# Optimization experiments

Hardware: AMD Instinct MI355X
Metric: run time of the kernel (lower is better)

The kernel has to match this reference:

```python
import jax, jax.numpy as jnp
import numpy as np

HEADS = 16
DIM = 1024
SPARSITY = 0.1


def setup_inputs() -> dict:
    key = jax.random.key(0)
    k1, k2, k3 = jax.random.split(key, 3)
    b, n, d = 2, 2048, DIM
    inner = HEADS * 64  # dim_head=64 -> inner_dim = 1024
    x = jax.random.normal(k1, (b, n, d), dtype=jnp.float32)
    W_qkv = jax.random.normal(k2, (3 * inner, d), dtype=jnp.float32) * (d ** -0.5)
    W_out = jax.random.normal(k3, (d, inner), dtype=jnp.float32) * (inner ** -0.5)
    b_out = jnp.zeros((d,), dtype=jnp.float32)
    return {"x": x, "W_qkv": W_qkv, "W_out": W_out, "b_out": b_out}


def reference(x, W_qkv, W_out, b_out):
    b, n, d = x.shape
    h = HEADS
    scale = d ** -0.5  # source uses dim**-0.5, not dim_head
    qkv = jnp.einsum('bnd,ed->bne', x, W_qkv)        # [b, n, 3*inner]
    q, k, v = jnp.split(qkv, 3, axis=-1)
    # b n (h dh) -> b h n dh
    def to_heads(t):
        return t.reshape(b, n, h, -1).transpose(0, 2, 1, 3)
    q, k, v = to_heads(q), to_heads(k), to_heads(v)
    dots = jnp.einsum('bhid,bhjd->bhij', q, k) * scale  # [b, h, n, n]
    mask_value = -jnp.finfo(dots.dtype).max
    k_top = max(1, int(SPARSITY * n))
    topk_vals, _ = jax.lax.top_k(dots, k_top)           # [b, h, n, k_top]
    thresh = topk_vals[..., -1:]                         # kth largest per row
    dots = jnp.where(dots >= thresh, dots, mask_value)   # keep ties, like torch
    v = jax.nn.relu(v)
    attn = jax.nn.softmax(dots, axis=-1)
    out = jnp.einsum('bhij,bhjd->bhid', attn, v)         # [b, h, n, dh]
    out = out.transpose(0, 2, 1, 3).reshape(b, n, -1)    # [b, n, inner]
    out = jnp.einsum('bne,de->bnd', out, W_out) + b_out  # to_out Linear (dropout=0)
    return out
```

## Files before the change

### kernel.cpp

```cpp
#include <hip/hip_runtime.h>


using f16x8 = __attribute__((ext_vector_type(8))) _Float16;
using u16x8 = __attribute__((ext_vector_type(8))) unsigned short;
using f32x4 = __attribute__((ext_vector_type(4))) float;

#define MFMA16F(a, b, c) __builtin_amdgcn_mfma_f32_16x16x32_f16(a, b, c, 0, 0, 0)

__device__ __forceinline__ unsigned short f2h(float f) {
  return __builtin_bit_cast(unsigned short, (_Float16)f);
}
__device__ __forceinline__ float h2f(unsigned int u) {
  return (float)__builtin_bit_cast(_Float16, (unsigned short)u);
}
__device__ __forceinline__ unsigned int key16(unsigned int u) {
  return (u & 0x8000u) ? (~u & 0xFFFFu) : (u | 0x8000u);
}
__device__ __forceinline__ unsigned int inv_key16(unsigned int k) {
  return (k & 0x8000u) ? (k & 0x7FFFu) : (~k & 0xFFFFu);
}
__device__ __forceinline__ float wred_sum(float v) {
#pragma unroll
  for (int off = 32; off > 0; off >>= 1) v += __shfl_xor(v, off);
  return v;
}

__device__ __forceinline__ int hist_select(const unsigned int* hw, int lane,
                                           int rank, int* cntAbove) {
  unsigned int S = hw[4 * lane] + hw[4 * lane + 1] + hw[4 * lane + 2] + hw[4 * lane + 3];
#pragma unroll
  for (int off = 1; off < 64; off <<= 1) {
    unsigned int v = (unsigned int)__shfl_down((int)S, off);
    if (lane + off < 64) S += v;
  }
  unsigned long long ball = __ballot((int)S >= rank);
  int lstar = 63 - __builtin_clzll(ball);
  unsigned int Sst = (unsigned int)__shfl((int)S, lstar);
  unsigned int h0 = hw[4 * lstar], h1 = hw[4 * lstar + 1];
  unsigned int h2 = hw[4 * lstar + 2], h3 = hw[4 * lstar + 3];
  unsigned int g = Sst - h0 - h1 - h2 - h3;
  int bb; unsigned int ca;
  if ((int)(g + h3) >= rank)                { bb = 4 * lstar + 3; ca = g; }
  else if ((int)(g + h3 + h2) >= rank)      { bb = 4 * lstar + 2; ca = g + h3; }
  else if ((int)(g + h3 + h2 + h1) >= rank) { bb = 4 * lstar + 1; ca = g + h3 + h2; }
  else                                      { bb = 4 * lstar;     ca = g + h3 + h2 + h1; }
  *cntAbove = (int)ca;
  return bb;
}

__global__ void cast_f32_f16(const float* __restrict__ s,
                             unsigned short* __restrict__ d, int n4, int scaleN4) {
  int i = blockIdx.x * blockDim.x + threadIdx.x;
  int stride = gridDim.x * blockDim.x;
  for (; i < n4; i += stride) {
    float4 v = ((const float4*)s)[i];
    float sc = (i < scaleN4) ? 0.03125f : 1.0f;
    ushort4 o;
    o.x = f2h(v.x * sc); o.y = f2h(v.y * sc); o.z = f2h(v.z * sc); o.w = f2h(v.w * sc);
    ((ushort4*)d)[i] = o;
  }
}

__global__ __launch_bounds__(256, 2) void gemm_qkv(
    const unsigned short* __restrict__ A, const unsigned short* __restrict__ W,
    unsigned short* __restrict__ out) {
  const int K = 1024;
  __shared__ unsigned short As[128 * 32];
  __shared__ unsigned short Bs[128 * 32];
  int t = threadIdx.x;
  int m0 = blockIdx.y * 128, n0 = blockIdx.x * 128;
  int lane = t & 63, wave = t >> 6;
  int wm = wave >> 1, wn = wave & 1;
  int rs = t >> 2, cs = t & 3;
  int cl = cs ^ ((rs >> 1) & 3);
  const unsigned short* pa0 = A + (size_t)(m0 + rs) * K + cl * 8;
  const unsigned short* pa1 = A + (size_t)(m0 + rs + 64) * K + cl * 8;
  const unsigned short* pb0 = W + (size_t)(n0 + rs) * K + cl * 8;
  const unsigned short* pb1 = W + (size_t)(n0 + rs + 64) * K + cl * 8;
  u16x8 ra0 = *(const u16x8*)pa0;
  u16x8 ra1 = *(const u16x8*)pa1;
  u16x8 rb0 = *(const u16x8*)pb0;
  u16x8 rb1 = *(const u16x8*)pb1;
  f32x4 zz = {0.f, 0.f, 0.f, 0.f};
  f32x4 acc[4][4];
#pragma unroll
  for (int i = 0; i < 4; ++i)
#pragma unroll
    for (int j = 0; j < 4; ++j) acc[i][j] = zz;
  int rr = lane & 15, cc = lane >> 4;
  int slot = (cc ^ ((rr >> 1) & 3)) * 8;
  for (int kt = 0; kt < K; kt += 32) {
    __syncthreads();
    *(u16x8*)&As[rs * 32 + cs * 8] = ra0;
    *(u16x8*)&As[(rs + 64) * 32 + cs * 8] = ra1;
    *(u16x8*)&Bs[rs * 32 + cs * 8] = rb0;
    *(u16x8*)&Bs[(rs + 64) * 32 + cs * 8] = rb1;
    if (kt + 32 < K) {
      ra0 = *(const u16x8*)(pa0 + kt + 32);
      ra1 = *(const u16x8*)(pa1 + kt + 32);
      rb0 = *(const u16x8*)(pb0 + kt + 32);
      rb1 = *(const u16x8*)(pb1 + kt + 32);
    }
    __syncthreads();
    f16x8 af[4], bfr[4];
#pragma unroll
    for (int f = 0; f < 4; ++f) {
      af[f]  = *(const f16x8*)&As[(wm * 64 + f * 16 + rr) * 32 + slot];
      bfr[f] = *(const f16x8*)&Bs[(wn * 64 + f * 16 + rr) * 32 + slot];
    }
#pragma unroll
    for (int fi = 0; fi < 4; ++fi)
#pragma unroll
      for (int fj = 0; fj < 4; ++fj)
        acc[fi][fj] = MFMA16F(bfr[fj], af[fi], acc[fi][fj]);
  }
#pragma unroll
  for (int fi = 0; fi < 4; ++fi) {
#pragma unroll
    for (int fj = 0; fj < 4; ++fj) {
      int m = m0 + wm * 64 + fi * 16 + rr;
      int n = n0 + wn * 64 + fj * 16 + cc * 4;
      ushort4 pk;
      pk.x = f2h(acc[fi][fj][0]); pk.y = f2h(acc[fi][fj][1]);
      pk.z = f2h(acc[fi][fj][2]); pk.w = f2h(acc[fi][fj][3]);
      *(ushort4*)&out[(size_t)m * 3072 + n] = pk;
    }
  }
}

__global__ __launch_bounds__(256) void vtrans(const unsigned short* __restrict__ qkv,
                                              unsigned short* __restrict__ vt) {
  __shared__ unsigned short tile[64][72];
  int q0 = blockIdx.x * 64;
  int bh = blockIdx.y;
  int b = bh >> 4, h = bh & 15;
  int t = threadIdx.x;
  int r = t >> 2, seg = t & 3;
  const unsigned short* src =
      qkv + (size_t)(b * 2048 + q0 + r) * 3072 + 2048 + h * 64 + seg * 16;
  *(u16x8*)&tile[r][seg * 16]     = *(const u16x8*)src;
  *(u16x8*)&tile[r][seg * 16 + 8] = *(const u16x8*)(src + 8);
  __syncthreads();
  int dh = t & 63, qs = t >> 6;
  unsigned short vals[16];
#pragma unroll
  for (int j = 0; j < 16; ++j) {
    unsigned short v = tile[qs * 16 + j][dh];
    vals[j] = (v & 0x8000) ? (unsigned short)0 : v;
  }
  unsigned short* dst = vt + (size_t)(bh * 64 + dh) * 2048 + q0 + qs * 16;
  *(u16x8*)&dst[0] = *(u16x8*)&vals[0];
  *(u16x8*)&dst[8] = *(u16x8*)&vals[8];
}

#define DSF 2068
__global__ __launch_bounds__(512, 4) void attn3(
    const unsigned short* __restrict__ qkv, const unsigned short* __restrict__ Vt,
    unsigned short* __restrict__ O) {
  __shared__ unsigned short dotsH[16 * DSF];
  __shared__ unsigned int hist[8][256];
  __shared__ float s_sh[16];
  __shared__ float out_sh[16 * 68];
  int L = blockIdx.x;
  int xcd = L & 7, idx = L >> 3;
  int bh = xcd * 4 + (idx >> 7);
  int q0 = (idx & 127) << 4;
  int b = bh >> 4, h = bh & 15;
  int t = threadIdx.x, lane = t & 63, wave = t >> 6;
  int rr = lane & 15, cc = lane >> 4;

  const unsigned short* qbase = qkv + (size_t)(b * 2048) * 3072 + h * 64;
  const unsigned short* kbase = qkv + (size_t)(b * 2048) * 3072 + 1024 + h * 64;
  const unsigned short* Vh = Vt + (size_t)bh * 64 * 2048;

  f16x8 aq0 = *(const f16x8*)(qbase + (size_t)(q0 + rr) * 3072 + cc * 8);
  f16x8 aq1 = *(const f16x8*)(qbase + (size_t)(q0 + rr) * 3072 + 32 + cc * 8);

  for (int i = t; i < 16 * 68; i += 512) out_sh[i] = 0.f;

#pragma unroll 2
  for (int jb = wave; jb < 128; jb += 8) {
    const unsigned short* kp = kbase + (size_t)(jb * 16 + rr) * 3072 + cc * 8;
    f16x8 kb0 = *(const f16x8*)(kp);
    f16x8 kb1 = *(const f16x8*)(kp + 32);
    f32x4 acc = {0.f, 0.f, 0.f, 0.f};
    acc = MFMA16F(kb0, aq0, acc);
    acc = MFMA16F(kb1, aq1, acc);
    ushort4 pk;
    pk.x = f2h(acc[0]); pk.y = f2h(acc[1]); pk.z = f2h(acc[2]); pk.w = f2h(acc[3]);
    *(ushort4*)&dotsH[rr * DSF + jb * 16 + cc * 4] = pk;
  }
  __syncthreads();

  const int KTOP = 204;
#pragma unroll 1
  for (int rw = 0; rw < 2; ++rw) {
    int row = wave * 2 + rw;
    const unsigned int* rp = (const unsigned int*)(dotsH + row * DSF);
    unsigned int bits[16];
#pragma unroll
    for (int k = 0; k < 16; ++k) bits[k] = rp[lane + 64 * k];
    unsigned int* hw = hist[wave];
#pragma unroll
    for (int i = 0; i < 4; ++i) hw[lane * 4 + i] = 0;
    int kmax = 0;
#pragma unroll
    for (int k = 0; k < 16; ++k) {
      unsigned int k0 = key16(bits[k] & 0xFFFFu);
      unsigned int k1 = key16(bits[k] >> 16);
      int kk = (int)(k0 > k1 ? k0 : k1);
      kmax = kmax > kk ? kmax : kk;
      atomicAdd(&hw[k0 >> 8], 1u);
      atomicAdd(&hw[k1 >> 8], 1u);
    }
    asm volatile("s_waitcnt lgkmcnt(0)" ::: "memory");
    int cntAbove1;
    int bstar = hist_select(hw, lane, KTOP, &cntAbove1);
    int rank2 = KTOP - cntAbove1;
#pragma unroll
    for (int i = 0; i < 4; ++i) hw[lane * 4 + i] = 0;
#pragma unroll
    for (int k = 0; k < 16; ++k) {
      unsigned int k0 = key16(bits[k] & 0xFFFFu);
      unsigned int k1 = key16(bits[k] >> 16);
      if ((int)(k0 >> 8) == bstar) atomicAdd(&hw[k0 & 255u], 1u);
      if ((int)(k1 >> 8) == bstar) atomicAdd(&hw[k1 & 255u], 1u);
    }
    asm volatile("s_waitcnt lgkmcnt(0)" ::: "memory");
    int cntAbove2;
    int b2 = hist_select(hw, lane, rank2, &cntAbove2);
    unsigned int thrKey = ((unsigned int)bstar << 8) | (unsigned int)b2;
#pragma unroll
    for (int off = 32; off > 0; off >>= 1) {
      int o = __shfl_xor(kmax, off);
      kmax = kmax > o ? kmax : o;
    }
    float vmax = h2f(inv_key16((unsigned int)kmax));
    float sum = 0.f;
    unsigned int* wp = (unsigned int*)(dotsH + row * DSF);
#pragma unroll
    for (int k = 0; k < 16; ++k) {
      unsigned int u0 = bits[k] & 0xFFFFu, u1 = bits[k] >> 16;
      unsigned int k0 = key16(u0), k1 = key16(u1);
      float p0 = (k0 >= thrKey) ? __expf(h2f(u0) - vmax) : 0.f;
      float p1 = (k1 >= thrKey) ? __expf(h2f(u1) - vmax) : 0.f;
      sum += p0 + p1;
      wp[lane + 64 * k] = (unsigned int)f2h(p0) | ((unsigned int)f2h(p1) << 16);
    }
    sum = wred_sum(sum);
    if (lane == 0) s_sh[row] = sum;
  }
  __syncthreads();

  f32x4 accp = {0.f, 0.f, 0.f, 0.f};
  int db = wave & 3;
  int js0 = (wave >> 2) * 32;
  const unsigned short* vrow = Vh + (size_t)(db * 16 + rr) * 2048;
#pragma unroll 4
  for (int js = js0; js < js0 + 32; ++js) {
    const unsigned short* pp = &dotsH[rr * DSF + js * 32 + cc * 8];
    uint2 lo = *(const uint2*)pp;
    uint2 hi = *(const uint2*)(pp + 4);
    uint4 tmp; tmp.x = lo.x; tmp.y = lo.y; tmp.z = hi.x; tmp.w = hi.y;
    f16x8 pa = __builtin_bit_cast(f16x8, tmp);
    f16x8 vb = *(const f16x8*)(vrow + js * 32 + cc * 8);
    accp = MFMA16F(pa, vb, accp);
  }
#pragma unroll
  for (int r = 0; r < 4; ++r) {
    int q = cc * 4 + r;
    atomicAdd(&out_sh[q * 68 + db * 16 + rr], accp[r]);
  }
  __syncthreads();

  for (int i = t; i < 1024; i += 512) {
    int q = i >> 6, d = i & 63;
    float v = out_sh[q * 68 + d] / s_sh[q];
    O[(size_t)(b * 2048 + q0 + q) * 1024 + h * 64 + d] = f2h(v);
  }
}

__global__ __launch_bounds__(256, 2) void gemm_out(
    const unsigned short* __restrict__ A, const unsigned short* __restrict__ W,
    const float* __restrict__ bias, float* __restrict__ out) {
  const int K = 1024;
  __shared__ unsigned short As[128 * 32];
  __shared__ unsigned short Bs[128 * 32];
  int t = threadIdx.x;
  int m0 = blockIdx.y * 128, n0 = blockIdx.x * 128;
  int lane = t & 63, wave = t >> 6;
  int wm = wave >> 1, wn = wave & 1;
  int rs = t >> 2, cs = t & 3;
  int cl = cs ^ ((rs >> 1) & 3);
  const unsigned short* pa0 = A + (size_t)(m0 + rs) * K + cl * 8;
  const unsigned short* pa1 = A + (size_t)(m0 + rs + 64) * K + cl * 8;
  const unsigned short* pb0 = W + (size_t)(n0 + rs) * K + cl * 8;
  const unsigned short* pb1 = W + (size_t)(n0 + rs + 64) * K + cl * 8;
  u16x8 ra0 = *(const u16x8*)pa0;
  u16x8 ra1 = *(const u16x8*)pa1;
  u16x8 rb0 = *(const u16x8*)pb0;
  u16x8 rb1 = *(const u16x8*)pb1;
  f32x4 zz = {0.f, 0.f, 0.f, 0.f};
  f32x4 acc[4][4];
#pragma unroll
  for (int i = 0; i < 4; ++i)
#pragma unroll
    for (int j = 0; j < 4; ++j) acc[i][j] = zz;
  int rr = lane & 15, cc = lane >> 4;
  int slot = (cc ^ ((rr >> 1) & 3)) * 8;
  for (int kt = 0; kt < K; kt += 32) {
    __syncthreads();
    *(u16x8*)&As[rs * 32 + cs * 8] = ra0;
    *(u16x8*)&As[(rs + 64) * 32 + cs * 8] = ra1;
    *(u16x8*)&Bs[rs * 32 + cs * 8] = rb0;
    *(u16x8*)&Bs[(rs + 64) * 32 + cs * 8] = rb1;
    if (kt + 32 < K) {
      ra0 = *(const u16x8*)(pa0 + kt + 32);
      ra1 = *(const u16x8*)(pa1 + kt + 32);
      rb0 = *(const u16x8*)(pb0 + kt + 32);
      rb1 = *(const u16x8*)(pb1 + kt + 32);
    }
    __syncthreads();
    f16x8 af[4], bfr[4];
#pragma unroll
    for (int f = 0; f < 4; ++f) {
      af[f]  = *(const f16x8*)&As[(wm * 64 + f * 16 + rr) * 32 + slot];
      bfr[f] = *(const f16x8*)&Bs[(wn * 64 + f * 16 + rr) * 32 + slot];
    }
#pragma unroll
    for (int fi = 0; fi < 4; ++fi)
#pragma unroll
      for (int fj = 0; fj < 4; ++fj)
        acc[fi][fj] = MFMA16F(bfr[fj], af[fi], acc[fi][fj]);
  }
#pragma unroll
  for (int fi = 0; fi < 4; ++fi) {
#pragma unroll
    for (int fj = 0; fj < 4; ++fj) {
      int m = m0 + wm * 64 + fi * 16 + rr;
      int n = n0 + wn * 64 + fj * 16 + cc * 4;
      f32x4 bv = *(const f32x4*)&bias[n];
      f32x4 o = acc[fi][fj] + bv;
      *(f32x4*)&out[(size_t)m * 1024 + n] = o;
    }
  }
}

extern "C" void kernel_launch(void* const* d_in, const int* in_sizes, int n_in,
                              void* d_out, int out_size, void* d_ws,
                              size_t ws_size, hipStream_t stream) {
  (void)in_sizes; (void)n_in; (void)out_size; (void)ws_size;
  const float* x    = (const float*)d_in[0];
  const float* Wqkv = (const float*)d_in[1];
  const float* Wout = (const float*)d_in[2];
  const float* bout = (const float*)d_in[3];
  float* out = (float*)d_out;

  char* ws = (char*)d_ws;
  unsigned short* x_h  = (unsigned short*)(ws);
  unsigned short* ao   = (unsigned short*)(ws);
  unsigned short* wq_h = (unsigned short*)(ws + 8388608);
  unsigned short* vt   = (unsigned short*)(ws + 8388608);
  unsigned short* wo_h = (unsigned short*)(ws + 16777216);
  unsigned short* qkv  = (unsigned short*)(ws + 18874368);

  cast_f32_f16<<<1024, 256, 0, stream>>>(x, x_h, 1048576, 0);
  cast_f32_f16<<<768, 256, 0, stream>>>(Wqkv, wq_h, 786432, 262144);
  cast_f32_f16<<<256, 256, 0, stream>>>(Wout, wo_h, 262144, 0);
  gemm_qkv<<<dim3(24, 32), 256, 0, stream>>>(x_h, wq_h, qkv);
  vtrans<<<dim3(32, 32), 256, 0, stream>>>(qkv, vt);
  attn3<<<4096, 512, 0, stream>>>(qkv, vt, ao);
  gemm_out<<<dim3(8, 32), 256, 0, stream>>>(ao, wo_h, bout, out);
}
```

Before: 447.0 us.

## Replace LDS histogram top-k threshold with bitwise radix search via ballot

```diff
diff --git a/kernel.cpp b/kernel.cpp
--- a/kernel.cpp
+++ b/kernel.cpp
@@ -23,29 +23,6 @@
 #pragma unroll
   for (int off = 32; off > 0; off >>= 1) v += __shfl_xor(v, off);
   return v;
-}
-
-__device__ __forceinline__ int hist_select(const unsigned int* hw, int lane,
-                                           int rank, int* cntAbove) {
-  unsigned int S = hw[4 * lane] + hw[4 * lane + 1] + hw[4 * lane + 2] + hw[4 * lane + 3];
-#pragma unroll
-  for (int off = 1; off < 64; off <<= 1) {
-    unsigned int v = (unsigned int)__shfl_down((int)S, off);
-    if (lane + off < 64) S += v;
-  }
-  unsigned long long ball = __ballot((int)S >= rank);
-  int lstar = 63 - __builtin_clzll(ball);
-  unsigned int Sst = (unsigned int)__shfl((int)S, lstar);
-  unsigned int h0 = hw[4 * lstar], h1 = hw[4 * lstar + 1];
-  unsigned int h2 = hw[4 * lstar + 2], h3 = hw[4 * lstar + 3];
-  unsigned int g = Sst - h0 - h1 - h2 - h3;
-  int bb; unsigned int ca;
-  if ((int)(g + h3) >= rank)                { bb = 4 * lstar + 3; ca = g; }
-  else if ((int)(g + h3 + h2) >= rank)      { bb = 4 * lstar + 2; ca = g + h3; }
-  else if ((int)(g + h3 + h2 + h1) >= rank) { bb = 4 * lstar + 1; ca = g + h3 + h2; }
-  else                                      { bb = 4 * lstar;     ca = g + h3 + h2 + h1; }
-  *cntAbove = (int)ca;
-  return bb;
 }
 
 __global__ void cast_f32_f16(const float* __restrict__ s,
@@ -154,11 +131,10 @@
 }
 
 #define DSF 2068
-__global__ __launch_bounds__(512, 4) void attn3(
+__global__ __launch_bounds__(512, 4) void attn4(
     const unsigned short* __restrict__ qkv, const unsigned short* __restrict__ Vt,
     unsigned short* __restrict__ O) {
   __shared__ unsigned short dotsH[16 * DSF];
-  __shared__ unsigned int hist[8][256];
   __shared__ float s_sh[16];
   __shared__ float out_sh[16 * 68];
   int L = blockIdx.x;
@@ -197,53 +173,40 @@
   for (int rw = 0; rw < 2; ++rw) {
     int row = wave * 2 + rw;
     const unsigned int* rp = (const unsigned int*)(dotsH + row * DSF);
-    unsigned int bits[16];
-#pragma unroll
-    for (int k = 0; k < 16; ++k) bits[k] = rp[lane + 64 * k];
-    unsigned int* hw = hist[wave];
-#pragma unroll
-    for (int i = 0; i < 4; ++i) hw[lane * 4 + i] = 0;
-    int kmax = 0;
+    unsigned int keys[32];
 #pragma unroll
     for (int k = 0; k < 16; ++k) {
-      unsigned int k0 = key16(bits[k] & 0xFFFFu);
-      unsigned int k1 = key16(bits[k] >> 16);
-      int kk = (int)(k0 > k1 ? k0 : k1);
-      kmax = kmax > kk ? kmax : kk;
-      atomicAdd(&hw[k0 >> 8], 1u);
-      atomicAdd(&hw[k1 >> 8], 1u);
-    }
-    asm volatile("s_waitcnt lgkmcnt(0)" ::: "memory");
-    int cntAbove1;
-    int bstar = hist_select(hw, lane, KTOP, &cntAbove1);
-    int rank2 = KTOP - cntAbove1;
-#pragma unroll
-    for (int i = 0; i < 4; ++i) hw[lane * 4 + i] = 0;
-#pragma unroll
-    for (int k = 0; k < 16; ++k) {
-      unsigned int k0 = key16(bits[k] & 0xFFFFu);
-      unsigned int k1 = key16(bits[k] >> 16);
-      if ((int)(k0 >> 8) == bstar) atomicAdd(&hw[k0 & 255u], 1u);
-      if ((int)(k1 >> 8) == bstar) atomicAdd(&hw[k1 & 255u], 1u);
-    }
-    asm volatile("s_waitcnt lgkmcnt(0)" ::: "memory");
-    int cntAbove2;
-    int b2 = hist_select(hw, lane, rank2, &cntAbove2);
-    unsigned int thrKey = ((unsigned int)bstar << 8) | (unsigned int)b2;
+      unsigned int w = rp[lane + 64 * k];
+      keys[2 * k]     = key16(w & 0xFFFFu);
+      keys[2 * k + 1] = key16(w >> 16);
+    }
+    unsigned int kmax = 0;
+#pragma unroll
+    for (int k = 0; k < 32; ++k) kmax = kmax > keys[k] ? kmax : keys[k];
 #pragma unroll
     for (int off = 32; off > 0; off >>= 1) {
-      int o = __shfl_xor(kmax, off);
+      unsigned int o = (unsigned int)__shfl_xor((int)kmax, off);
       kmax = kmax > o ? kmax : o;
     }
-    float vmax = h2f(inv_key16((unsigned int)kmax));
+    unsigned int cur = 0;
+#pragma unroll 1
+    for (int bit = 15; bit >= 0; --bit) {
+      unsigned int cand = cur | (1u << bit);
+      int cnt = 0;
+#pragma unroll
+      for (int k = 0; k < 32; ++k)
+        cnt += __popcll(__ballot(keys[k] >= cand));
+      if (cnt >= KTOP) cur = cand;
+    }
+    unsigned int thrKey = cur;
+    float vmax = h2f(inv_key16(kmax));
     float sum = 0.f;
     unsigned int* wp = (unsigned int*)(dotsH + row * DSF);
 #pragma unroll
     for (int k = 0; k < 16; ++k) {
-      unsigned int u0 = bits[k] & 0xFFFFu, u1 = bits[k] >> 16;
-      unsigned int k0 = key16(u0), k1 = key16(u1);
-      float p0 = (k0 >= thrKey) ? __expf(h2f(u0) - vmax) : 0.f;
-      float p1 = (k1 >= thrKey) ? __expf(h2f(u1) - vmax) : 0.f;
+      unsigned int k0 = keys[2 * k], k1 = keys[2 * k + 1];
+      float p0 = (k0 >= thrKey) ? __expf(h2f(inv_key16(k0)) - vmax) : 0.f;
+      float p1 = (k1 >= thrKey) ? __expf(h2f(inv_key16(k1)) - vmax) : 0.f;
       sum += p0 + p1;
       wp[lane + 64 * k] = (unsigned int)f2h(p0) | ((unsigned int)f2h(p1) << 16);
     }
@@ -369,6 +332,6 @@
   cast_f32_f16<<<256, 256, 0, stream>>>(Wout, wo_h, 262144, 0);
   gemm_qkv<<<dim3(24, 32), 256, 0, stream>>>(x_h, wq_h, qkv);
   vtrans<<<dim3(32, 32), 256, 0, stream>>>(qkv, vt);
-  attn3<<<4096, 512, 0, stream>>>(qkv, vt, ao);
+  attn4<<<4096, 512, 0, stream>>>(qkv, vt, ao);
   gemm_out<<<dim3(8, 32), 256, 0, stream>>>(ao, wo_h, bout, out);
 }
```

After: 483.6 us. 8.2% more time.
